# Optimization experiments

Hardware: AMD Instinct MI355X
Metric: run time of the kernel (lower is better)

The kernel has to match this reference:

```python
import jax, jax.numpy as jnp
import numpy as np

N = 50000
E = 640000
H = 128
C = 3

def _xavier(key, shape, gain=1.0):
    fan_in, fan_out = shape[0], shape[1]
    a = gain * np.sqrt(6.0 / (fan_in + fan_out))
    return jax.random.uniform(key, shape, jnp.float32, -a, a)

def setup_inputs() -> dict:
    key = jax.random.key(0)
    ks = jax.random.split(key, 12)
    h = jax.random.normal(ks[0], (N, H), jnp.float32)
    x = jax.random.normal(ks[1], (N, C), jnp.float32)
    edge_index = jax.random.randint(ks[2], (2, E), 0, N, jnp.int64 if jax.config.jax_enable_x64 else jnp.int32)
    # edge_mlp: Linear(2H+1 -> H), SiLU, Linear(H -> H), SiLU
    We1 = _xavier(ks[3], (2 * H + 1, H)); be1 = jnp.zeros((H,), jnp.float32)
    We2 = _xavier(ks[4], (H, H));          be2 = jnp.zeros((H,), jnp.float32)
    # coord_mlp: Linear(H -> H), SiLU, Linear(H -> 1, no bias, gain 0.01)
    Wc1 = _xavier(ks[5], (H, H)); bc1 = jnp.zeros((H,), jnp.float32)
    Wc2 = _xavier(ks[6], (H, 1), gain=0.01)
    # node_mlp: Linear(2H -> H), SiLU, Linear(H -> H)
    Wn1 = _xavier(ks[7], (2 * H, H)); bn1 = jnp.zeros((H,), jnp.float32)
    Wn2 = _xavier(ks[8], (H, H));     bn2 = jnp.zeros((H,), jnp.float32)
    return dict(h=h, x=x, edge_index=edge_index,
                We1=We1, be1=be1, We2=We2, be2=be2,
                Wc1=Wc1, bc1=bc1, Wc2=Wc2,
                Wn1=Wn1, bn1=bn1, Wn2=Wn2, bn2=bn2)

def reference(h, x, edge_index, We1, be1, We2, be2, Wc1, bc1, Wc2, Wn1, bn1, Wn2, bn2):
    src, dst = edge_index[0], edge_index[1]
    n = h.shape[0]
    rel_pos = x[src] - x[dst]                              # [E, C]
    dist_sq = jnp.sum(rel_pos * rel_pos, axis=-1, keepdims=True)  # [E, 1]
    edge_input = jnp.concatenate([h[src], h[dst], dist_sq], axis=-1)  # [E, 2H+1]
    m_ij = jax.nn.silu(edge_input @ We1 + be1)
    m_ij = jax.nn.silu(m_ij @ We2 + be2)                   # [E, H]
    coord_weight = jax.nn.silu(m_ij @ Wc1 + bc1) @ Wc2     # [E, 1]
    coord_agg = jax.ops.segment_sum(rel_pos * coord_weight, dst, num_segments=n)
    x_out = x + coord_agg
    msg_agg = jax.ops.segment_sum(m_ij, dst, num_segments=n)  # [N, H]
    node_input = jnp.concatenate([h, msg_agg], axis=-1)    # [N, 2H]
    h_upd = jax.nn.silu(node_input @ Wn1 + bn1) @ Wn2 + bn2
    h_out = h + h_upd
    return (h_out, x_out)
```

## Files before the change

### kernel.cpp

```cpp
#include <hip/hip_runtime.h>

#define H 128

typedef __bf16 bf8_t __attribute__((ext_vector_type(8)));
typedef float  f4_t  __attribute__((ext_vector_type(4)));

#define MFMA16(a, b, c) __builtin_amdgcn_mfma_f32_16x16x32_bf16((a), (b), (c), 0, 0, 0)

__device__ __forceinline__ float silu_f(float v) {
    return v * (1.0f / (1.0f + __expf(-v)));
}

__device__ __forceinline__ void bar_lds() {
    asm volatile("s_waitcnt lgkmcnt(0)\ns_barrier" ::: "memory");
}

__device__ __forceinline__ float wload(const void* p, int idx, bool f32) {
    return f32 ? ((const float*)p)[idx] : (float)((const __bf16*)p)[idx];
}

__device__ __forceinline__ bf8_t hload8(const void* p, size_t off, bool f32) {
    bf8_t v;
    if (f32) {
        const float4* q = (const float4*)((const float*)p + off);
        const float4 a = q[0], b = q[1];
        v[0]=(__bf16)a.x; v[1]=(__bf16)a.y; v[2]=(__bf16)a.z; v[3]=(__bf16)a.w;
        v[4]=(__bf16)b.x; v[5]=(__bf16)b.y; v[6]=(__bf16)b.z; v[7]=(__bf16)b.w;
    } else {
        v = *(const bf8_t*)((const __bf16*)p + off);
    }
    return v;
}

__device__ __forceinline__ int eidx(const void* ei, int i, bool i64) {
    return i64 ? (int)((const long long*)ei)[i] : ((const int*)ei)[i];
}

__global__ void detect_kernel(const unsigned short* __restrict__ hraw,
                              const int* __restrict__ eiraw, int* __restrict__ flags)
{
    __shared__ int s_nf, s_oddnz;
    if (threadIdx.x == 0) { s_nf = 0; s_oddnz = 0; }
    __syncthreads();
    int nf = 0;
    for (int i = threadIdx.x; i < 16384; i += blockDim.x) {
        const unsigned short u = hraw[i];
        if (((u >> 7) & 0xFF) == 0xFF) nf++;
    }
    int onz = 0;
    for (int i = threadIdx.x; i < 512; i += blockDim.x) {
        if (eiraw[2*i + 1] != 0) onz++;
    }
    if (nf)  atomicAdd(&s_nf, nf);
    if (onz) atomicAdd(&s_oddnz, onz);
    __syncthreads();
    if (threadIdx.x == 0) {
        flags[0] = (s_nf > 0) ? 1 : 0;
        flags[1] = (s_oddnz == 0) ? 1 : 0;
    }
}

__global__ void histd_kernel(const void* __restrict__ ei, int* __restrict__ cnt,
                             const int* __restrict__ flags, int Ee)
{
    const int e = blockIdx.x*blockDim.x + threadIdx.x;
    if (e < Ee) atomicAdd(&cnt[eidx(ei, Ee + e, flags[1] != 0)], 1);
}

__global__ void scanA_kernel(const int* __restrict__ cnt, int* __restrict__ bsum, int Nn)
{
    __shared__ int s[512];
    const int gi = blockIdx.x*512 + threadIdx.x;
    s[threadIdx.x] = (gi < Nn) ? cnt[gi] : 0;
    __syncthreads();
    for (int off = 256; off > 0; off >>= 1) {
        if (threadIdx.x < off) s[threadIdx.x] += s[threadIdx.x + off];
        __syncthreads();
    }
    if (threadIdx.x == 0) bsum[blockIdx.x] = s[0];
}

__global__ void scanB_kernel(int* __restrict__ bsum, int* __restrict__ base, int nCh)
{
    if (threadIdx.x == 0) {
        int acc = 0;
        for (int b = 0; b < nCh; ++b) { base[b] = acc; acc += bsum[b]; }
    }
}

__global__ void scanC_kernel(const int* __restrict__ cnt, const int* __restrict__ base,
                             int* __restrict__ off, int* __restrict__ cursor, int Nn)
{
    __shared__ int s[512];
    const int i  = threadIdx.x;
    const int gi = blockIdx.x*512 + i;
    const int v  = (gi < Nn) ? cnt[gi] : 0;
    s[i] = v;
    __syncthreads();
    for (int o = 1; o < 512; o <<= 1) {
        const int t = (i >= o) ? s[i - o] : 0;
        __syncthreads();
        s[i] += t;
        __syncthreads();
    }
    const int excl = s[i] - v;
    if (gi <= Nn) {
        const int val = base[blockIdx.x] + excl;
        off[gi] = val;
        if (gi < Nn) cursor[gi] = val;
    }
}

__global__ void scatgeo_kernel(const void* __restrict__ ei, int* __restrict__ cursor,
                               int* __restrict__ srcs, int* __restrict__ dsts,
                               float* __restrict__ d2buf, const void* __restrict__ x,
                               const int* __restrict__ flags, int Ee)
{
    const int e = blockIdx.x*blockDim.x + threadIdx.x;
    if (e >= Ee) return;
    const bool i64 = flags[1] != 0;
    const bool f32 = flags[0] != 0;
    const int s = eidx(ei, e, i64);
    const int d = eidx(ei, Ee + e, i64);
    const int p = atomicAdd(&cursor[d], 1);
    srcs[p] = s;
    dsts[p] = d;
    float d2 = 0.f;
    #pragma unroll
    for (int c = 0; c < 3; ++c) {
        const float r = wload(x, s*3 + c, f32) - wload(x, d*3 + c, f32);
        d2 += r*r;
    }
    d2buf[p] = d2;
}

__global__ __launch_bounds__(512, 2)
void proj_kernel(const void* __restrict__ h, const void* __restrict__ We1,
                 const void* __restrict__ be1, const int* __restrict__ flags,
                 __bf16* __restrict__ PB, int Nn)
{
    const bool f32 = flags[0] != 0;
    const int tid  = threadIdx.x;
    const int wv   = tid >> 6;
    const int lane = tid & 63;
    const int quad = lane >> 4;
    const int l15  = lane & 15;

    bf8_t bW[4][2];
    float bias[2];
    #pragma unroll
    for (int t = 0; t < 2; ++t) {
        const int n    = wv*32 + t*16 + l15;
        const int rb   = (n < 128) ? 0 : 128;
        const int col  = n & 127;
        #pragma unroll
        for (int kc = 0; kc < 4; ++kc) {
            bf8_t v;
            #pragma unroll
            for (int j = 0; j < 8; ++j)
                v[j] = (__bf16)wload(We1, (rb + kc*32 + quad*8 + j)*H + col, f32);
            bW[kc][t] = v;
        }
        bias[t] = (n < 128) ? 0.f : wload(be1, col, f32);
    }

    __shared__ __bf16 s_h[32*136];

    const int tiles = (Nn + 31) >> 5;
    for (int tile = blockIdx.x; tile < tiles; tile += gridDim.x) {
        const int nb = tile << 5;
        __syncthreads();
        {
            const int m = tid >> 4, c = tid & 15;
            int node = nb + m; if (node >= Nn) node = Nn - 1;
            *(bf8_t*)&s_h[m*136 + c*8] = hload8(h, (size_t)node*H + c*8, f32);
        }
        __syncthreads();

        f4_t acc[2][2];
        #pragma unroll
        for (int mm = 0; mm < 2; ++mm)
            #pragma unroll
            for (int t = 0; t < 2; ++t) acc[mm][t] = (f4_t){0.f,0.f,0.f,0.f};
        #pragma unroll
        for (int kc = 0; kc < 4; ++kc) {
            #pragma unroll
            for (int mm = 0; mm < 2; ++mm) {
                const bf8_t a = *(const bf8_t*)&s_h[(mm*16 + l15)*136 + quad*8 + kc*32];
                acc[mm][0] = MFMA16(a, bW[kc][0], acc[mm][0]);
                acc[mm][1] = MFMA16(a, bW[kc][1], acc[mm][1]);
            }
        }
        #pragma unroll
        for (int mm = 0; mm < 2; ++mm)
            #pragma unroll
            for (int i = 0; i < 4; ++i) {
                const int row = nb + mm*16 + quad*4 + i;
                if (row < Nn) {
                    #pragma unroll
                    for (int t = 0; t < 2; ++t)
                        PB[(size_t)row*256 + wv*32 + t*16 + l15] =
                            (__bf16)(acc[mm][t][i] + bias[t]);
                }
            }
    }
}

__global__ __launch_bounds__(512, 2)
void egnn_edge_pipe_kernel(const __bf16* __restrict__ PB,
                           const int* __restrict__ srcs, const int* __restrict__ dsts,
                           const float* __restrict__ d2buf,
                           const void* __restrict__ We1,
                           const void* __restrict__ We2, const void* __restrict__ be2,
                           const void* __restrict__ Wc1, const void* __restrict__ bc1,
                           const void* __restrict__ Wc2, const int* __restrict__ flags,
                           __bf16* __restrict__ m_buf, float* __restrict__ cw_buf,
                           int Ee)
{
    const bool f32 = flags[0] != 0;
    const int tid  = threadIdx.x;
    const int wv   = tid >> 6;
    const int lane = tid & 63;
    const int quad = lane >> 4;
    const int l15  = lane & 15;
    const int mg   = wv >> 2;
    const int ng   = wv & 3;

    bf8_t bW2[4][2], bWc[4][2];
    float be2v[2], bc1v[2], wc2v[2];
    #pragma unroll
    for (int t = 0; t < 2; ++t) {
        const int n = ng*32 + t*16 + l15;
        #pragma unroll
        for (int kc = 0; kc < 4; ++kc) {
            bf8_t v, u;
            #pragma unroll
            for (int j = 0; j < 8; ++j) {
                v[j] = (__bf16)wload(We2, (kc*32 + quad*8 + j)*H + n, f32);
                u[j] = (__bf16)wload(Wc1, (kc*32 + quad*8 + j)*H + n, f32);
            }
            bW2[kc][t] = v;
            bWc[kc][t] = u;
        }
        be2v[t] = wload(be2, n, f32);
        bc1v[t] = wload(bc1, n, f32);
        wc2v[t] = wload(Wc2, n, f32);
    }

    const int em = tid >> 3;
    const int ch = tid & 7;
    float w1dA[8], w1dB[8];
    #pragma unroll
    for (int j = 0; j < 8; ++j) {
        w1dA[j] = wload(We1, 256*H + ch*8 + j, f32);
        w1dB[j] = wload(We1, 256*H + (ch+8)*8 + j, f32);
    }

    __shared__ __bf16 s_m1[64*136];
    __shared__ __bf16 s_m2[64*136];
    __shared__ float  s_cw[64*4];

    const int tiles = (Ee + 63) >> 6;

    bf8_t rA0, rA1, rB0, rB1;
    float d2cur;
    int   s_n, d_n;
    float d2nxt;
    {
        int e0 = blockIdx.x*64 + em; if (e0 >= Ee) e0 = Ee - 1;
        const int sc = srcs[e0], dc = dsts[e0];
        d2cur = d2buf[e0];
        rA0 = *(const bf8_t*)(PB + (size_t)sc*256 + ch*8);
        rA1 = *(const bf8_t*)(PB + (size_t)sc*256 + (ch+8)*8);
        rB0 = *(const bf8_t*)(PB + (size_t)dc*256 + 128 + ch*8);
        rB1 = *(const bf8_t*)(PB + (size_t)dc*256 + 128 + (ch+8)*8);
        const int t1 = blockIdx.x + gridDim.x;
        const int tt = (t1 < tiles) ? t1 : blockIdx.x;
        int e1 = tt*64 + em; if (e1 >= Ee) e1 = Ee - 1;
        s_n = srcs[e1]; d_n = dsts[e1]; d2nxt = d2buf[e1];
    }

    for (int t = blockIdx.x; t < tiles; t += gridDim.x) {
        {
            bf8_t o0, o1;
            #pragma unroll
            for (int j = 0; j < 8; ++j) {
                const float f0 = (float)rA0[j] + (float)rB0[j] + d2cur*w1dA[j];
                const float f1 = (float)rA1[j] + (float)rB1[j] + d2cur*w1dB[j];
                o0[j] = (__bf16)silu_f(f0);
                o1[j] = (__bf16)silu_f(f1);
            }
            *(bf8_t*)&s_m1[em*136 + ch*8]       = o0;
            *(bf8_t*)&s_m1[em*136 + (ch+8)*8]   = o1;
        }
        {
            const int sc = s_n, dc = d_n;
            rA0 = *(const bf8_t*)(PB + (size_t)sc*256 + ch*8);
            rA1 = *(const bf8_t*)(PB + (size_t)sc*256 + (ch+8)*8);
            rB0 = *(const bf8_t*)(PB + (size_t)dc*256 + 128 + ch*8);
            rB1 = *(const bf8_t*)(PB + (size_t)dc*256 + 128 + (ch+8)*8);
            d2cur = d2nxt;
            const int t2 = t + 2*gridDim.x;
            const int tt = (t2 < tiles) ? t2 : t;
            int e2 = tt*64 + em; if (e2 >= Ee) e2 = Ee - 1;
            s_n = srcs[e2]; d_n = dsts[e2]; d2nxt = d2buf[e2];
        }
        bar_lds();

        {
            f4_t a2[2][2];
            #pragma unroll
            for (int mm = 0; mm < 2; ++mm)
                #pragma unroll
                for (int h2 = 0; h2 < 2; ++h2) a2[mm][h2] = (f4_t){0.f,0.f,0.f,0.f};
            #pragma unroll
            for (int kc = 0; kc < 4; ++kc) {
                #pragma unroll
                for (int mm = 0; mm < 2; ++mm) {
                    const bf8_t a = *(const bf8_t*)&s_m1[(mg*32 + mm*16 + l15)*136 + quad*8 + kc*32];
                    a2[mm][0] = MFMA16(a, bW2[kc][0], a2[mm][0]);
                    a2[mm][1] = MFMA16(a, bW2[kc][1], a2[mm][1]);
                }
            }
            #pragma unroll
            for (int mm = 0; mm < 2; ++mm)
                #pragma unroll
                for (int i = 0; i < 4; ++i) {
                    const int m = mg*32 + mm*16 + quad*4 + i;
                    s_m2[m*136 + ng*32 + l15]      = (__bf16)silu_f(a2[mm][0][i] + be2v[0]);
                    s_m2[m*136 + ng*32 + 16 + l15] = (__bf16)silu_f(a2[mm][1][i] + be2v[1]);
                }
        }
        bar_lds();

        {
            const int ms = tid >> 4, c2 = tid & 15;
            *(bf8_t*)(m_buf + ((size_t)t*64 + ms)*H + c2*8) =
                *(const bf8_t*)&s_m2[ms*136 + c2*8];
            *(bf8_t*)(m_buf + ((size_t)t*64 + 32 + ms)*H + c2*8) =
                *(const bf8_t*)&s_m2[(ms+32)*136 + c2*8];
        }

        {
            f4_t a3[2][2];
            #pragma unroll
            for (int mm = 0; mm < 2; ++mm)
                #pragma unroll
                for (int h2 = 0; h2 < 2; ++h2) a3[mm][h2] = (f4_t){0.f,0.f,0.f,0.f};
            #pragma unroll
            for (int kc = 0; kc < 4; ++kc) {
                #pragma unroll
                for (int mm = 0; mm < 2; ++mm) {
                    const bf8_t a = *(const bf8_t*)&s_m2[(mg*32 + mm*16 + l15)*136 + quad*8 + kc*32];
                    a3[mm][0] = MFMA16(a, bWc[kc][0], a3[mm][0]);
                    a3[mm][1] = MFMA16(a, bWc[kc][1], a3[mm][1]);
                }
            }
            float p[2][4];
            #pragma unroll
            for (int mm = 0; mm < 2; ++mm)
                #pragma unroll
                for (int i = 0; i < 4; ++i) {
                    const float v0 = silu_f(a3[mm][0][i] + bc1v[0]);
                    const float v1 = silu_f(a3[mm][1][i] + bc1v[1]);
                    p[mm][i] = v0*wc2v[0] + v1*wc2v[1];
                }
            #pragma unroll
            for (int off = 1; off < 16; off <<= 1)
                #pragma unroll
                for (int mm = 0; mm < 2; ++mm)
                    #pragma unroll
                    for (int i = 0; i < 4; ++i) p[mm][i] += __shfl_xor(p[mm][i], off, 64);
            if (l15 == 0) {
                #pragma unroll
                for (int mm = 0; mm < 2; ++mm)
                    #pragma unroll
                    for (int i = 0; i < 4; ++i)
                        s_cw[(mg*32 + mm*16 + quad*4 + i)*4 + ng] = p[mm][i];
            }
        }
        bar_lds();

        if (tid < 64)
            cw_buf[(size_t)t*64 + tid] =
                s_cw[tid*4] + s_cw[tid*4+1] + s_cw[tid*4+2] + s_cw[tid*4+3];
    }
}

__global__ __launch_bounds__(512)
void egnn_agg_kernel(const void* __restrict__ x, const int* __restrict__ off,
                     const int* __restrict__ srcs, const __bf16* __restrict__ m_buf,
                     const float* __restrict__ cw_buf, float* __restrict__ msg_agg,
                     const int* __restrict__ flags, void* __restrict__ out,
                     size_t obase, int Nn)
{
    const bool f32 = flags[0] != 0;
    const int wv = threadIdx.x >> 6, lane = threadIdx.x & 63;
    const int n = blockIdx.x*8 + wv;
    if (n >= Nn) return;
    const int p0 = off[n], p1 = off[n+1];

    float xd0, xd1, xd2;
    if (f32) { const float* xp = (const float*)x + (size_t)n*3; xd0=xp[0]; xd1=xp[1]; xd2=xp[2]; }
    else     { const __bf16* xp = (const __bf16*)x + (size_t)n*3; xd0=(float)xp[0]; xd1=(float)xp[1]; xd2=(float)xp[2]; }

    float ms0 = 0.f, ms1 = 0.f, c0 = 0.f, c1 = 0.f, c2 = 0.f;
    const unsigned int* mb = (const unsigned int*)m_buf;
    for (int p = p0; p < p1; ++p) {
        const unsigned int u = mb[(size_t)p*64 + lane];
        ms0 += __uint_as_float(u << 16);
        ms1 += __uint_as_float(u & 0xffff0000u);
        const float cw = cw_buf[p];
        const int sn = srcs[p];
        float xs0, xs1, xs2;
        if (f32) { const float* xp = (const float*)x + (size_t)sn*3; xs0=xp[0]; xs1=xp[1]; xs2=xp[2]; }
        else     { const __bf16* xp = (const __bf16*)x + (size_t)sn*3; xs0=(float)xp[0]; xs1=(float)xp[1]; xs2=(float)xp[2]; }
        c0 += (xs0 - xd0)*cw;
        c1 += (xs1 - xd1)*cw;
        c2 += (xs2 - xd2)*cw;
    }
    float2 st; st.x = ms0; st.y = ms1;
    *(float2*)&msg_agg[(size_t)n*H + 2*lane] = st;
    if (lane == 0) {
        const float o0 = xd0 + c0, o1 = xd1 + c1, o2 = xd2 + c2;
        if (f32) {
            float* op = (float*)out + obase + (size_t)n*3;
            op[0] = o0; op[1] = o1; op[2] = o2;
        } else {
            __bf16* op = (__bf16*)out + obase + (size_t)n*3;
            op[0] = (__bf16)o0; op[1] = (__bf16)o1; op[2] = (__bf16)o2;
        }
    }
}

__global__ __launch_bounds__(512, 2)
void egnn_node_kernel(const void* __restrict__ h, const float* __restrict__ msg_agg,
                      const void* __restrict__ Wn1, const void* __restrict__ bn1,
                      const void* __restrict__ Wn2, const void* __restrict__ bn2,
                      const int* __restrict__ flags, void* __restrict__ h_out, int Nn)
{
    const bool f32 = flags[0] != 0;
    const int tid  = threadIdx.x;
    const int wv   = tid >> 6;
    const int lane = tid & 63;
    const int quad = lane >> 4;
    const int l15  = lane & 15;
    const int mg   = wv >> 2;
    const int ng   = wv & 3;

    bf8_t bW1[8][2];
    bf8_t bW2[4][2];
    float b1v[2], b2v[2];
    #pragma unroll
    for (int t = 0; t < 2; ++t) {
        const int n = ng*32 + t*16 + l15;
        #pragma unroll
        for (int kc = 0; kc < 8; ++kc) {
            bf8_t v;
            #pragma unroll
            for (int j = 0; j < 8; ++j) v[j] = (__bf16)wload(Wn1, (kc*32 + quad*8 + j)*H + n, f32);
            bW1[kc][t] = v;
        }
        #pragma unroll
        for (int kc = 0; kc < 4; ++kc) {
            bf8_t v;
            #pragma unroll
            for (int j = 0; j < 8; ++j) v[j] = (__bf16)wload(Wn2, (kc*32 + quad*8 + j)*H + n, f32);
            bW2[kc][t] = v;
        }
        b1v[t] = wload(bn1, n, f32);
        b2v[t] = wload(bn2, n, f32);
    }

    __shared__ __bf16 s_in[32*264];
    __shared__ __bf16 s_t1[32*136];

    const int tiles = (Nn + 31) >> 5;
    for (int tile = blockIdx.x; tile < tiles; tile += gridDim.x) {
        const int nb = tile << 5;
        __syncthreads();
        #pragma unroll
        for (int r = 0; r < 2; ++r) {
            const int idx = tid + r*512;
            const int m = idx >> 5, c = idx & 31;
            int node = nb + m;
            if (node >= Nn) node = Nn - 1;
            if (c < 16) {
                *(bf8_t*)&s_in[m*264 + c*8] = hload8(h, (size_t)node*H + c*8, f32);
            } else {
                const float4* mp = (const float4*)(msg_agg + (size_t)node*H + (c - 16)*8);
                const float4 v0 = mp[0], v1 = mp[1];
                __bf16* d = &s_in[m*264 + c*8];
                d[0] = (__bf16)v0.x; d[1] = (__bf16)v0.y; d[2] = (__bf16)v0.z; d[3] = (__bf16)v0.w;
                d[4] = (__bf16)v1.x; d[5] = (__bf16)v1.y; d[6] = (__bf16)v1.z; d[7] = (__bf16)v1.w;
            }
        }
        __syncthreads();

        {
            f4_t a0 = {0.f,0.f,0.f,0.f}, a1 = {0.f,0.f,0.f,0.f};
            const int abase = (mg*16 + l15)*264 + quad*8;
            #pragma unroll
            for (int kc = 0; kc < 8; ++kc) {
                const bf8_t a = *(const bf8_t*)&s_in[abase + kc*32];
                a0 = MFMA16(a, bW1[kc][0], a0);
                a1 = MFMA16(a, bW1[kc][1], a1);
            }
            #pragma unroll
            for (int i = 0; i < 4; ++i) {
                const int m = mg*16 + quad*4 + i;
                s_t1[m*136 + ng*32 + l15]      = (__bf16)silu_f(a0[i] + b1v[0]);
                s_t1[m*136 + ng*32 + 16 + l15] = (__bf16)silu_f(a1[i] + b1v[1]);
            }
        }
        __syncthreads();

        {
            f4_t a0 = {0.f,0.f,0.f,0.f}, a1 = {0.f,0.f,0.f,0.f};
            const int abase = (mg*16 + l15)*136 + quad*8;
            #pragma unroll
            for (int kc = 0; kc < 4; ++kc) {
                const bf8_t a = *(const bf8_t*)&s_t1[abase + kc*32];
                a0 = MFMA16(a, bW2[kc][0], a0);
                a1 = MFMA16(a, bW2[kc][1], a1);
            }
            #pragma unroll
            for (int i = 0; i < 4; ++i) {
                const int node = nb + mg*16 + quad*4 + i;
                if (node < Nn) {
                    const int n0 = ng*32 + l15, n1 = n0 + 16;
                    const size_t i0 = (size_t)node*H + n0, i1 = (size_t)node*H + n1;
                    const float h0 = f32 ? ((const float*)h)[i0] : (float)((const __bf16*)h)[i0];
                    const float h1 = f32 ? ((const float*)h)[i1] : (float)((const __bf16*)h)[i1];
                    const float o0 = a0[i] + b2v[0] + h0;
                    const float o1 = a1[i] + b2v[1] + h1;
                    if (f32) {
                        ((float*)h_out)[i0] = o0;
                        ((float*)h_out)[i1] = o1;
                    } else {
                        ((__bf16*)h_out)[i0] = (__bf16)o0;
                        ((__bf16*)h_out)[i1] = (__bf16)o1;
                    }
                }
            }
        }
    }
}

__global__ void cvt_ei_kernel(const void* __restrict__ src, int* __restrict__ dst,
                              int n, const int* __restrict__ flags)
{
    const int i = blockIdx.x*blockDim.x + threadIdx.x;
    if (i >= n) return;
    dst[i] = flags[1] ? (int)((const long long*)src)[i] : ((const int*)src)[i];
}

__global__ __launch_bounds__(512, 2)
void egnn_edge_kernel(const void* __restrict__ h, const void* __restrict__ x,
                      const int* __restrict__ ei,
                      const void* __restrict__ We1, const void* __restrict__ be1,
                      const void* __restrict__ We2, const void* __restrict__ be2,
                      const void* __restrict__ Wc1, const void* __restrict__ bc1,
                      const void* __restrict__ Wc2, const int* __restrict__ flags,
                      float* __restrict__ msg_agg, float* __restrict__ coord_agg,
                      int Nn, int Ee)
{
    const bool f32 = flags[0] != 0;
    const int tid  = threadIdx.x;
    const int wv   = tid >> 6;
    const int lane = tid & 63;
    const int quad = lane >> 4;
    const int l15  = lane & 15;
    const int mg   = wv >> 2;
    const int ng   = wv & 3;

    bf8_t bW1[8][2];
    bf8_t bW2[4][2];
    bf8_t bWc[4][2];
    float be1v[2], be2v[2], bc1v[2], w1dv[2], wc2v[2];
    #pragma unroll
    for (int t = 0; t < 2; ++t) {
        const int n = ng*32 + t*16 + l15;
        #pragma unroll
        for (int kc = 0; kc < 8; ++kc) {
            bf8_t v;
            #pragma unroll
            for (int j = 0; j < 8; ++j) v[j] = (__bf16)wload(We1, (kc*32 + quad*8 + j)*H + n, f32);
            bW1[kc][t] = v;
        }
        #pragma unroll
        for (int kc = 0; kc < 4; ++kc) {
            bf8_t v, u;
            #pragma unroll
            for (int j = 0; j < 8; ++j) {
                v[j] = (__bf16)wload(We2, (kc*32 + quad*8 + j)*H + n, f32);
                u[j] = (__bf16)wload(Wc1, (kc*32 + quad*8 + j)*H + n, f32);
            }
            bW2[kc][t] = v;
            bWc[kc][t] = u;
        }
        be1v[t] = wload(be1, n, f32);
        be2v[t] = wload(be2, n, f32);
        bc1v[t] = wload(bc1, n, f32);
        w1dv[t] = wload(We1, 256*H + n, f32);
        wc2v[t] = wload(Wc2, n, f32);
    }

    __shared__ __bf16 s_in[32*264];
    __shared__ __bf16 s_m1[32*136];
    __shared__ __bf16 s_m2[32*136];
    __shared__ float  s_rel[32*3];
    __shared__ float  s_dist[32];
    __shared__ int    s_dstv[32];
    __shared__ float  s_cw[32*4];

    const int tiles = Ee >> 5;
    for (int tile = blockIdx.x; tile < tiles; tile += gridDim.x) {
        const int ebase = tile << 5;
        __syncthreads();

        if (tid < 32) {
            const int e  = ebase + tid;
            const int sn = ei[e];
            const int dn = ei[Ee + e];
            s_dstv[tid] = dn;
            float d2 = 0.f;
            #pragma unroll
            for (int c = 0; c < 3; ++c) {
                float r;
                if (f32) r = ((const float*)x)[sn*3 + c] - ((const float*)x)[dn*3 + c];
                else     r = (float)((const __bf16*)x)[sn*3 + c] - (float)((const __bf16*)x)[dn*3 + c];
                s_rel[tid*3 + c] = r;
                d2 += r*r;
            }
            s_dist[tid] = d2;
        }
        #pragma unroll
        for (int r = 0; r < 2; ++r) {
            const int idx = tid + r*512;
            const int m = idx >> 5, c = idx & 31;
            const int e = ebase + m;
            const int node = (c < 16) ? ei[e] : ei[Ee + e];
            *(bf8_t*)&s_in[m*264 + c*8] = hload8(h, (size_t)node*H + (c & 15)*8, f32);
        }
        __syncthreads();

        {
            f4_t a0 = {0.f,0.f,0.f,0.f}, a1 = {0.f,0.f,0.f,0.f};
            const int abase = (mg*16 + l15)*264 + quad*8;
            #pragma unroll
            for (int kc = 0; kc < 8; ++kc) {
                const bf8_t a = *(const bf8_t*)&s_in[abase + kc*32];
                a0 = MFMA16(a, bW1[kc][0], a0);
                a1 = MFMA16(a, bW1[kc][1], a1);
            }
            #pragma unroll
            for (int i = 0; i < 4; ++i) {
                const int m = mg*16 + quad*4 + i;
                const float d2 = s_dist[m];
                s_m1[m*136 + ng*32 + l15]      = (__bf16)silu_f(a0[i] + d2*w1dv[0] + be1v[0]);
                s_m1[m*136 + ng*32 + 16 + l15] = (__bf16)silu_f(a1[i] + d2*w1dv[1] + be1v[1]);
            }
        }
        __syncthreads();

        {
            f4_t a0 = {0.f,0.f,0.f,0.f}, a1 = {0.f,0.f,0.f,0.f};
            const int abase = (mg*16 + l15)*136 + quad*8;
            #pragma unroll
            for (int kc = 0; kc < 4; ++kc) {
                const bf8_t a = *(const bf8_t*)&s_m1[abase + kc*32];
                a0 = MFMA16(a, bW2[kc][0], a0);
                a1 = MFMA16(a, bW2[kc][1], a1);
            }
            #pragma unroll
            for (int i = 0; i < 4; ++i) {
                const int m = mg*16 + quad*4 + i;
                const float v0 = silu_f(a0[i] + be2v[0]);
                const float v1 = silu_f(a1[i] + be2v[1]);
                s_m2[m*136 + ng*32 + l15]      = (__bf16)v0;
                s_m2[m*136 + ng*32 + 16 + l15] = (__bf16)v1;
                const size_t db = (size_t)s_dstv[m]*H + ng*32 + l15;
                atomicAdd(&msg_agg[db],      v0);
                atomicAdd(&msg_agg[db + 16], v1);
            }
        }
        __syncthreads();

        {
            f4_t a0 = {0.f,0.f,0.f,0.f}, a1 = {0.f,0.f,0.f,0.f};
            const int abase = (mg*16 + l15)*136 + quad*8;
            #pragma unroll
            for (int kc = 0; kc < 4; ++kc) {
                const bf8_t a = *(const bf8_t*)&s_m2[abase + kc*32];
                a0 = MFMA16(a, bWc[kc][0], a0);
                a1 = MFMA16(a, bWc[kc][1], a1);
            }
            float p[4];
            #pragma unroll
            for (int i = 0; i < 4; ++i) {
                const float v0 = silu_f(a0[i] + bc1v[0]);
                const float v1 = silu_f(a1[i] + bc1v[1]);
                p[i] = v0*wc2v[0] + v1*wc2v[1];
            }
            #pragma unroll
            for (int off = 1; off < 16; off <<= 1) {
                #pragma unroll
                for (int i = 0; i < 4; ++i) p[i] += __shfl_xor(p[i], off, 64);
            }
            if (l15 == 0) {
                #pragma unroll
                for (int i = 0; i < 4; ++i)
                    s_cw[(mg*16 + quad*4 + i)*4 + ng] = p[i];
            }
        }
        __syncthreads();

        if (tid < 96) {
            const int m = tid / 3, c = tid - m*3;
            const float cw = s_cw[m*4 + 0] + s_cw[m*4 + 1] + s_cw[m*4 + 2] + s_cw[m*4 + 3];
            atomicAdd(&coord_agg[(size_t)s_dstv[m]*3 + c], s_rel[m*3 + c]*cw);
        }
    }
}

__global__ void egnn_x_kernel(const void* __restrict__ x, const float* __restrict__ coord_agg,
                              const int* __restrict__ flags, void* __restrict__ out,
                              size_t obase, int total)
{
    const bool f32 = flags[0] != 0;
    const int i = blockIdx.x*blockDim.x + threadIdx.x;
    if (i >= total) return;
    const float xv = f32 ? ((const float*)x)[i] : (float)((const __bf16*)x)[i];
    const float o = xv + coord_agg[i];
    if (f32) ((float*)out)[obase + i] = o;
    else     ((__bf16*)out)[obase + i] = (__bf16)o;
}

static inline size_t align256(size_t v) { return (v + 255) & ~(size_t)255; }

extern "C" void kernel_launch(void* const* d_in, const int* in_sizes, int n_in,
                              void* d_out, int out_size, void* d_ws, size_t ws_size,
                              hipStream_t stream)
{
    const void* h   = d_in[0];
    const void* x   = d_in[1];
    const void* ei0 = d_in[2];
    const void* We1 = d_in[3];
    const void* be1 = d_in[4];
    const void* We2 = d_in[5];
    const void* be2 = d_in[6];
    const void* Wc1 = d_in[7];
    const void* bc1 = d_in[8];
    const void* Wc2 = d_in[9];
    const void* Wn1 = d_in[10];
    const void* bn1 = d_in[11];
    const void* Wn2 = d_in[12];
    const void* bn2 = d_in[13];

    const int Nn = in_sizes[0] / H;
    const int Ee = in_sizes[2] / 2;
    const int EeP = ((Ee + 63) & ~63) + 64;

    char* ws = (char*)d_ws;
    size_t o = 0;
    size_t o_mbuf  = o; o = align256(o + (size_t)EeP*H*2);
    size_t o_msg   = o; o = align256(o + (size_t)Nn*H*4);
    size_t o_srcs  = o; o = align256(o + (size_t)Ee*4);
    size_t o_dsts  = o; o = align256(o + (size_t)Ee*4);
    size_t o_cw    = o; o = align256(o + (size_t)EeP*4);
    size_t o_d2    = o; o = align256(o + (size_t)Ee*4);
    size_t o_pb    = o; o = align256(o + (size_t)Nn*256*2);
    size_t o_cnt   = o; o = align256(o + (size_t)Nn*4);
    size_t o_off   = o; o = align256(o + (size_t)(Nn+1)*4);
    size_t o_cur   = o; o = align256(o + (size_t)Nn*4);
    size_t o_bsum  = o; o = align256(o + 512*4);
    size_t o_base  = o; o = align256(o + 512*4);
    size_t o_flags = o; o = align256(o + 64);
    const size_t need_csr = o;

    const int nCh = (Nn + 1 + 511) / 512;

    if (ws_size >= need_csr) {
        __bf16* m_buf   = (__bf16*)(ws + o_mbuf);
        float*  msg_agg = (float*) (ws + o_msg);
        int*    srcs    = (int*)   (ws + o_srcs);
        int*    dsts    = (int*)   (ws + o_dsts);
        float*  cw_buf  = (float*) (ws + o_cw);
        float*  d2buf   = (float*) (ws + o_d2);
        __bf16* PB      = (__bf16*)(ws + o_pb);
        int*    cnt     = (int*)   (ws + o_cnt);
        int*    off     = (int*)   (ws + o_off);
        int*    cursor  = (int*)   (ws + o_cur);
        int*    bsum    = (int*)   (ws + o_bsum);
        int*    base    = (int*)   (ws + o_base);
        int*    flags   = (int*)   (ws + o_flags);

        detect_kernel<<<1, 256, 0, stream>>>((const unsigned short*)h, (const int*)ei0, flags);
        hipMemsetAsync(cnt, 0, (size_t)Nn*4, stream);
        histd_kernel<<<(Ee + 511)/512, 512, 0, stream>>>(ei0, cnt, flags, Ee);
        scanA_kernel<<<nCh, 512, 0, stream>>>(cnt, bsum, Nn);
        scanB_kernel<<<1, 64, 0, stream>>>(bsum, base, nCh);
        scanC_kernel<<<nCh, 512, 0, stream>>>(cnt, base, off, cursor, Nn);
        scatgeo_kernel<<<(Ee + 511)/512, 512, 0, stream>>>(ei0, cursor, srcs, dsts,
                                                           d2buf, x, flags, Ee);
        proj_kernel<<<512, 512, 0, stream>>>(h, We1, be1, flags, PB, Nn);

        egnn_edge_pipe_kernel<<<512, 512, 0, stream>>>(PB, srcs, dsts, d2buf,
                                                       We1, We2, be2, Wc1, bc1, Wc2,
                                                       flags, m_buf, cw_buf, Ee);

        egnn_agg_kernel<<<(Nn + 7)/8, 512, 0, stream>>>(x, off, srcs, m_buf, cw_buf,
                                                        msg_agg, flags, d_out, (size_t)Nn*H, Nn);
        egnn_node_kernel<<<512, 512, 0, stream>>>(h, msg_agg, Wn1, bn1, Wn2, bn2,
                                                  flags, d_out, Nn);
    } else {
        float* msg_agg   = (float*)ws;
        float* coord_agg = (float*)(ws + (size_t)Nn*H*4);
        int*   ei        = (int*)  (ws + (size_t)Nn*H*4 + (size_t)Nn*3*4);
        int*   flags     = (int*)  (ws + (size_t)Nn*H*4 + (size_t)Nn*3*4 + (size_t)2*Ee*4);

        detect_kernel<<<1, 256, 0, stream>>>((const unsigned short*)h, (const int*)ei0, flags);
        cvt_ei_kernel<<<(2*Ee + 255)/256, 256, 0, stream>>>(ei0, ei, 2*Ee, flags);
        hipMemsetAsync(msg_agg,   0, (size_t)Nn*H*4, stream);
        hipMemsetAsync(coord_agg, 0, (size_t)Nn*3*4, stream);
        egnn_edge_kernel<<<1024, 512, 0, stream>>>(h, x, ei, We1, be1, We2, be2,
                                                   Wc1, bc1, Wc2, flags,
                                                   msg_agg, coord_agg, Nn, Ee);
        egnn_node_kernel<<<512, 512, 0, stream>>>(h, msg_agg, Wn1, bn1, Wn2, bn2,
                                                  flags, d_out, Nn);
        egnn_x_kernel<<<(Nn*3 + 255)/256, 256, 0, stream>>>(x, coord_agg, flags, d_out,
                                                            (size_t)Nn*H, Nn*3);
    }
}
```

Before: 686.4 us.

## Precompute relative positions, store bf16 message aggregate, double grid sizes

The scatter kernel now writes each edge's relative position and squared distance as a float4 in CSR order. The aggregation kernel can then read these contiguously instead of gathering x[src] through srcs. The aggregated messages are stored as bf16 instead of fp32, which halves their write and read traffic and lets the node kernel load them directly as bf16 vectors. The persistent proj, edge and node kernels also go from 512 to 1024 blocks. This adds a 16-byte-per-edge buffer and an extra write in the scatter pass, and the bf16 rounding of msg_agg happens earlier (the node kernel already converted it to bf16 in LDS).

```diff
diff --git a/kernel.cpp b/kernel.cpp
--- a/kernel.cpp
+++ b/kernel.cpp
@@ -113,7 +113,8 @@
 
 __global__ void scatgeo_kernel(const void* __restrict__ ei, int* __restrict__ cursor,
                                int* __restrict__ srcs, int* __restrict__ dsts,
-                               float* __restrict__ d2buf, const void* __restrict__ x,
+                               float* __restrict__ d2buf, float4* __restrict__ rel4,
+                               const void* __restrict__ x,
                                const int* __restrict__ flags, int Ee)
 {
     const int e = blockIdx.x*blockDim.x + threadIdx.x;
@@ -125,13 +126,14 @@
     const int p = atomicAdd(&cursor[d], 1);
     srcs[p] = s;
     dsts[p] = d;
-    float d2 = 0.f;
+    float r[3];
     #pragma unroll
-    for (int c = 0; c < 3; ++c) {
-        const float r = wload(x, s*3 + c, f32) - wload(x, d*3 + c, f32);
-        d2 += r*r;
-    }
+    for (int c = 0; c < 3; ++c)
+        r[c] = wload(x, s*3 + c, f32) - wload(x, d*3 + c, f32);
+    const float d2 = r[0]*r[0] + r[1]*r[1] + r[2]*r[2];
     d2buf[p] = d2;
+    float4 o; o.x = r[0]; o.y = r[1]; o.z = r[2]; o.w = d2;
+    rel4[p] = o;
 }
 
 __global__ __launch_bounds__(512, 2)
@@ -389,8 +391,8 @@
 
 __global__ __launch_bounds__(512)
 void egnn_agg_kernel(const void* __restrict__ x, const int* __restrict__ off,
-                     const int* __restrict__ srcs, const __bf16* __restrict__ m_buf,
-                     const float* __restrict__ cw_buf, float* __restrict__ msg_agg,
+                     const __bf16* __restrict__ m_buf, const float* __restrict__ cw_buf,
+                     const float4* __restrict__ rel4, __bf16* __restrict__ msgb,
                      const int* __restrict__ flags, void* __restrict__ out,
                      size_t obase, int Nn)
 {
@@ -399,10 +401,6 @@
     const int n = blockIdx.x*8 + wv;
     if (n >= Nn) return;
     const int p0 = off[n], p1 = off[n+1];
-
-    float xd0, xd1, xd2;
-    if (f32) { const float* xp = (const float*)x + (size_t)n*3; xd0=xp[0]; xd1=xp[1]; xd2=xp[2]; }
-    else     { const __bf16* xp = (const __bf16*)x + (size_t)n*3; xd0=(float)xp[0]; xd1=(float)xp[1]; xd2=(float)xp[2]; }
 
     float ms0 = 0.f, ms1 = 0.f, c0 = 0.f, c1 = 0.f, c2 = 0.f;
     const unsigned int* mb = (const unsigned int*)m_buf;
@@ -411,17 +409,16 @@
         ms0 += __uint_as_float(u << 16);
         ms1 += __uint_as_float(u & 0xffff0000u);
         const float cw = cw_buf[p];
-        const int sn = srcs[p];
-        float xs0, xs1, xs2;
-        if (f32) { const float* xp = (const float*)x + (size_t)sn*3; xs0=xp[0]; xs1=xp[1]; xs2=xp[2]; }
-        else     { const __bf16* xp = (const __bf16*)x + (size_t)sn*3; xs0=(float)xp[0]; xs1=(float)xp[1]; xs2=(float)xp[2]; }
-        c0 += (xs0 - xd0)*cw;
-        c1 += (xs1 - xd1)*cw;
-        c2 += (xs2 - xd2)*cw;
-    }
-    float2 st; st.x = ms0; st.y = ms1;
-    *(float2*)&msg_agg[(size_t)n*H + 2*lane] = st;
+        const float4 r = rel4[p];
+        c0 += r.x*cw; c1 += r.y*cw; c2 += r.z*cw;
+    }
+    union { unsigned int u; __bf16 b[2]; } pk;
+    pk.b[0] = (__bf16)ms0; pk.b[1] = (__bf16)ms1;
+    *(unsigned int*)&msgb[(size_t)n*H + 2*lane] = pk.u;
     if (lane == 0) {
+        float xd0, xd1, xd2;
+        if (f32) { const float* xp = (const float*)x + (size_t)n*3; xd0=xp[0]; xd1=xp[1]; xd2=xp[2]; }
+        else     { const __bf16* xp = (const __bf16*)x + (size_t)n*3; xd0=(float)xp[0]; xd1=(float)xp[1]; xd2=(float)xp[2]; }
         const float o0 = xd0 + c0, o1 = xd1 + c1, o2 = xd2 + c2;
         if (f32) {
             float* op = (float*)out + obase + (size_t)n*3;
@@ -434,10 +431,11 @@
 }
 
 __global__ __launch_bounds__(512, 2)
-void egnn_node_kernel(const void* __restrict__ h, const float* __restrict__ msg_agg,
+void egnn_node_kernel(const void* __restrict__ h, const void* __restrict__ msg,
                       const void* __restrict__ Wn1, const void* __restrict__ bn1,
                       const void* __restrict__ Wn2, const void* __restrict__ bn2,
-                      const int* __restrict__ flags, void* __restrict__ h_out, int Nn)
+                      const int* __restrict__ flags, void* __restrict__ h_out,
+                      int Nn, int msg_f32)
 {
     const bool f32 = flags[0] != 0;
     const int tid  = threadIdx.x;
@@ -487,12 +485,15 @@
             if (node >= Nn) node = Nn - 1;
             if (c < 16) {
                 *(bf8_t*)&s_in[m*264 + c*8] = hload8(h, (size_t)node*H + c*8, f32);
-            } else {
-                const float4* mp = (const float4*)(msg_agg + (size_t)node*H + (c - 16)*8);
+            } else if (msg_f32) {
+                const float4* mp = (const float4*)((const float*)msg + (size_t)node*H + (c - 16)*8);
                 const float4 v0 = mp[0], v1 = mp[1];
                 __bf16* d = &s_in[m*264 + c*8];
                 d[0] = (__bf16)v0.x; d[1] = (__bf16)v0.y; d[2] = (__bf16)v0.z; d[3] = (__bf16)v0.w;
                 d[4] = (__bf16)v1.x; d[5] = (__bf16)v1.y; d[6] = (__bf16)v1.z; d[7] = (__bf16)v1.w;
+            } else {
+                *(bf8_t*)&s_in[m*264 + c*8] =
+                    *(const bf8_t*)((const __bf16*)msg + (size_t)node*H + (c - 16)*8);
             }
         }
         __syncthreads();
@@ -765,11 +766,12 @@
     char* ws = (char*)d_ws;
     size_t o = 0;
     size_t o_mbuf  = o; o = align256(o + (size_t)EeP*H*2);
-    size_t o_msg   = o; o = align256(o + (size_t)Nn*H*4);
+    size_t o_msg   = o; o = align256(o + (size_t)Nn*H*2);
     size_t o_srcs  = o; o = align256(o + (size_t)Ee*4);
     size_t o_dsts  = o; o = align256(o + (size_t)Ee*4);
     size_t o_cw    = o; o = align256(o + (size_t)EeP*4);
     size_t o_d2    = o; o = align256(o + (size_t)Ee*4);
+    size_t o_rel   = o; o = align256(o + (size_t)Ee*16);
     size_t o_pb    = o; o = align256(o + (size_t)Nn*256*2);
     size_t o_cnt   = o; o = align256(o + (size_t)Nn*4);
     size_t o_off   = o; o = align256(o + (size_t)(Nn+1)*4);
@@ -783,11 +785,12 @@
 
     if (ws_size >= need_csr) {
         __bf16* m_buf   = (__bf16*)(ws + o_mbuf);
-        float*  msg_agg = (float*) (ws + o_msg);
+        __bf16* msgb    = (__bf16*)(ws + o_msg);
         int*    srcs    = (int*)   (ws + o_srcs);
         int*    dsts    = (int*)   (ws + o_dsts);
         float*  cw_buf  = (float*) (ws + o_cw);
         float*  d2buf   = (float*) (ws + o_d2);
+        float4* rel4    = (float4*)(ws + o_rel);
         __bf16* PB      = (__bf16*)(ws + o_pb);
         int*    cnt     = (int*)   (ws + o_cnt);
         int*    off     = (int*)   (ws + o_off);
@@ -803,17 +806,17 @@
         scanB_kernel<<<1, 64, 0, stream>>>(bsum, base, nCh);
         scanC_kernel<<<nCh, 512, 0, stream>>>(cnt, base, off, cursor, Nn);
         scatgeo_kernel<<<(Ee + 511)/512, 512, 0, stream>>>(ei0, cursor, srcs, dsts,
-                                                           d2buf, x, flags, Ee);
-        proj_kernel<<<512, 512, 0, stream>>>(h, We1, be1, flags, PB, Nn);
-
-        egnn_edge_pipe_kernel<<<512, 512, 0, stream>>>(PB, srcs, dsts, d2buf,
-                                                       We1, We2, be2, Wc1, bc1, Wc2,
-                                                       flags, m_buf, cw_buf, Ee);
-
-        egnn_agg_kernel<<<(Nn + 7)/8, 512, 0, stream>>>(x, off, srcs, m_buf, cw_buf,
-                                                        msg_agg, flags, d_out, (size_t)Nn*H, Nn);
-        egnn_node_kernel<<<512, 512, 0, stream>>>(h, msg_agg, Wn1, bn1, Wn2, bn2,
-                                                  flags, d_out, Nn);
+                                                           d2buf, rel4, x, flags, Ee);
+        proj_kernel<<<1024, 512, 0, stream>>>(h, We1, be1, flags, PB, Nn);
+
+        egnn_edge_pipe_kernel<<<1024, 512, 0, stream>>>(PB, srcs, dsts, d2buf,
+                                                        We1, We2, be2, Wc1, bc1, Wc2,
+                                                        flags, m_buf, cw_buf, Ee);
+
+        egnn_agg_kernel<<<(Nn + 7)/8, 512, 0, stream>>>(x, off, m_buf, cw_buf, rel4,
+                                                        msgb, flags, d_out, (size_t)Nn*H, Nn);
+        egnn_node_kernel<<<1024, 512, 0, stream>>>(h, msgb, Wn1, bn1, Wn2, bn2,
+                                                   flags, d_out, Nn, 0);
     } else {
         float* msg_agg   = (float*)ws;
         float* coord_agg = (float*)(ws + (size_t)Nn*H*4);
@@ -828,7 +831,7 @@
                                                    Wc1, bc1, Wc2, flags,
                                                    msg_agg, coord_agg, Nn, Ee);
         egnn_node_kernel<<<512, 512, 0, stream>>>(h, msg_agg, Wn1, bn1, Wn2, bn2,
-                                                  flags, d_out, Nn);
+                                                  flags, d_out, Nn, 1);
         egnn_x_kernel<<<(Nn*3 + 255)/256, 256, 0, stream>>>(x, coord_agg, flags, d_out,
                                                             (size_t)Nn*H, Nn*3);
     }
```

Result: slower. 752.1 us (+9.6%).
